# Performance work log

Hardware: AMD Instinct MI355X
Metric: run time of the kernel (lower is better)

## Reference

```python
import jax, jax.numpy as jnp
import numpy as np
import math

L, C, H, FF, V, T, B = 12, 768, 12, 3072, 50257, 512, 4
D = C // H  # head dim = 64


def _layernorm(x, w, b, eps=1e-5):
    m = x.mean(-1, keepdims=True)
    v = ((x - m) ** 2).mean(-1, keepdims=True)
    return (x - m) / jnp.sqrt(v + eps) * w + b


def _gelu(x):
    # tanh-approximate GELU exactly as in the torch module
    return 0.5 * x * (1.0 + jnp.tanh(math.sqrt(2.0 / math.pi) * (x + 0.044715 * x ** 3)))


def setup_inputs() -> dict:
    key = jax.random.key(0)
    ks = jax.random.split(key, 12)
    std = 0.02
    proj_std = 0.02 / math.sqrt(2 * L)
    inp = {
        "idx": jax.random.randint(ks[0], (B, T), 0, V),
        "targets": jax.random.randint(ks[1], (B, T), 0, V),
        "wte": jax.random.normal(ks[2], (V, C), jnp.float32) * std,
        "wpe": jax.random.normal(ks[3], (T, C), jnp.float32) * std,
        "ln1_w": jnp.ones((L, C), jnp.float32),
        "ln1_b": jnp.zeros((L, C), jnp.float32),
        "attn_w": jax.random.normal(ks[4], (L, C, 3 * C), jnp.float32) * std,
        "attn_b": jnp.zeros((L, 3 * C), jnp.float32),
        "attnp_w": jax.random.normal(ks[5], (L, C, C), jnp.float32) * proj_std,
        "attnp_b": jnp.zeros((L, C), jnp.float32),
        "ln2_w": jnp.ones((L, C), jnp.float32),
        "ln2_b": jnp.zeros((L, C), jnp.float32),
        "fc_w": jax.random.normal(ks[6], (L, C, FF), jnp.float32) * std,
        "fc_b": jnp.zeros((L, FF), jnp.float32),
        "fcp_w": jax.random.normal(ks[7], (L, FF, C), jnp.float32) * proj_std,
        "fcp_b": jnp.zeros((L, C), jnp.float32),
        "lnf_w": jnp.ones((C,), jnp.float32),
        "lnf_b": jnp.zeros((C,), jnp.float32),
        "lm_w": jax.random.normal(ks[8], (C, V), jnp.float32) * std,  # lm_head.weight.T
    }
    return inp


def _gpt_forward(idx, targets, wte, wpe, ln1_w, ln1_b, attn_w, attn_b,
                 attnp_w, attnp_b, ln2_w, ln2_b, fc_w, fc_b, fcp_w, fcp_b,
                 lnf_w, lnf_b, lm_w):
    b, t = idx.shape
    x = wte[idx] + wpe[:t][None]  # [B,T,C]
    causal = jnp.tril(jnp.ones((t, t), bool))  # [T,T]
    neg_inf = jnp.float32(-jnp.inf)

    def block(x, p):
        l1w, l1b, aw, ab, pw, pb, l2w, l2b, fw, fb, qw, qb = p
        h = _layernorm(x, l1w, l1b)
        qkv = h @ aw + ab  # [B,T,3C]
        q, k, v = jnp.split(qkv, 3, axis=-1)
        q = q.reshape(b, t, H, D).transpose(0, 2, 1, 3)  # [B,H,T,D]
        k = k.reshape(b, t, H, D).transpose(0, 2, 1, 3)
        v = v.reshape(b, t, H, D).transpose(0, 2, 1, 3)
        att = jnp.einsum('bhqd,bhkd->bhqk', q, k) * (1.0 / math.sqrt(D))
        att = jnp.where(causal, att, neg_inf)
        att = jax.nn.softmax(att, axis=-1)
        y = jnp.einsum('bhqk,bhkd->bhqd', att, v)  # [B,H,T,D]
        y = y.transpose(0, 2, 1, 3).reshape(b, t, C)
        x = x + (y @ pw + pb)
        h2 = _layernorm(x, l2w, l2b)
        x = x + (_gelu(h2 @ fw + fb) @ qw + qb)
        return x, None

    params = (ln1_w, ln1_b, attn_w, attn_b, attnp_w, attnp_b,
              ln2_w, ln2_b, fc_w, fc_b, fcp_w, fcp_b)
    x, _ = jax.lax.scan(block, x, params)
    x = _layernorm(x, lnf_w, lnf_b)
    logits = x @ lm_w  # [B,T,V]

    # cross_entropy with ignore_index=-100
    logp = jax.nn.log_softmax(logits, axis=-1)
    tgt = targets.reshape(-1)
    valid = (tgt != -100)
    safe_tgt = jnp.where(valid, tgt, 0)
    nll = -jnp.take_along_axis(logp.reshape(-1, logits.shape[-1]),
                               safe_tgt[:, None], axis=1)[:, 0]
    loss = jnp.sum(nll * valid) / jnp.maximum(jnp.sum(valid), 1)
    return logits, loss


def reference(idx, targets, wte, wpe, ln1_w, ln1_b, attn_w, attn_b,
              attnp_w, attnp_b, ln2_w, ln2_b, fc_w, fc_b, fcp_w, fcp_b,
              lnf_w, lnf_b, lm_w):
    return _gpt_forward(idx, targets, wte, wpe, ln1_w, ln1_b, attn_w, attn_b,
                        attnp_w, attnp_b, ln2_w, ln2_b, fc_w, fc_b,
                        fcp_w, fcp_b, lnf_w, lnf_b, lm_w)
```

## Files before the change

kernel.cpp:

```cpp
#include <hip/hip_runtime.h>
#include <hip/hip_bf16.h>
#include <math.h>

#define L_ 12
#define C_ 768
#define H_ 12
#define FF_ 3072
#define V_ 50257
#define VP2_ 50432
#define T_ 512
#define B_ 4
#define D_ 64
#define M_ (B_*T_)
#define BH_ (B_*H_)
#define NPAN_LM 197

typedef __attribute__((ext_vector_type(8))) short short8;
typedef __attribute__((ext_vector_type(4))) float f32x4;
typedef __attribute__((ext_vector_type(8))) unsigned short us8;
typedef __attribute__((ext_vector_type(4))) unsigned short us4;

__device__ __forceinline__ float bf2f(unsigned short u) {
    return __uint_as_float(((unsigned)u) << 16);
}
__device__ __forceinline__ unsigned short f2bf(float f) {
    unsigned u = __float_as_uint(f);
    unsigned r = u + 0x7fff + ((u >> 16) & 1);
    return (unsigned short)(r >> 16);
}

__device__ __forceinline__ void transpose_tile(
    const float* __restrict__ W, __hip_bfloat16* __restrict__ WT,
    int K, int N, int Npad, int bx, int by, int bz)
{
    __shared__ float tile[64][65];
    const float* Wl = W + (size_t)bz * K * N;
    __hip_bfloat16* WTl = WT + (size_t)bz * Npad * K;
    int k0 = by * 64, n0 = bx * 64;
    int tid = threadIdx.x;
    int tn = tid & 63, tk4 = tid >> 6;
#pragma unroll 4
    for (int i = 0; i < 16; ++i) {
        int k = tk4 * 16 + i;
        int n = n0 + tn;
        tile[k][tn] = (n < N) ? Wl[(size_t)(k0 + k) * N + n] : 0.f;
    }
    __syncthreads();
#pragma unroll
    for (int i = 0; i < 2; ++i) {
        int p = tid + i * 256;
        int n = p >> 3;
        int k8 = (p & 7) * 8;
        us8 v;
#pragma unroll
        for (int e = 0; e < 8; ++e) v[e] = f2bf(tile[k8 + e][n]);
        *(us8*)((unsigned short*)WTl + (size_t)(n0 + n) * K + k0 + k8) = v;
    }
}

__global__ __launch_bounds__(256) void transpose_all_kernel(
    const float* W0, __hip_bfloat16* T0,
    const float* W1, __hip_bfloat16* T1,
    const float* W2, __hip_bfloat16* T2,
    const float* W3, __hip_bfloat16* T3,
    const float* W4, __hip_bfloat16* T4)
{
    int bid = blockIdx.x;
    if (bid < 5184) {
        int bx = bid % 36, r = bid / 36;
        transpose_tile(W0, T0, C_, 3 * C_, 3 * C_, bx, r % 12, r / 12);
    } else if (bid < 6912) {
        int lb = bid - 5184;
        int bx = lb % 12, r = lb / 12;
        transpose_tile(W1, T1, C_, C_, C_, bx, r % 12, r / 12);
    } else if (bid < 13824) {
        int lb = bid - 6912;
        int bx = lb % 48, r = lb / 48;
        transpose_tile(W2, T2, C_, FF_, FF_, bx, r % 12, r / 12);
    } else if (bid < 20736) {
        int lb = bid - 13824;
        int bx = lb % 12, r = lb / 12;
        transpose_tile(W3, T3, FF_, C_, C_, bx, r % 48, r / 48);
    } else {
        int lb = bid - 20736;
        int bx = lb % 788, by = lb / 788;
        transpose_tile(W4, T4, C_, V_, VP2_, bx, by, 0);
    }
}

__global__ __launch_bounds__(256) void embed_kernel(
    const int* __restrict__ idx, const float* __restrict__ wte,
    const float* __restrict__ wpe, float* __restrict__ x, int total4)
{
    int i = blockIdx.x * blockDim.x + threadIdx.x;
    if (i >= total4) return;
    const int CQ = C_ / 4;
    int c4 = (i % CQ) * 4;
    int row = i / CQ;
    int t = row % T_;
    f32x4 a = *(const f32x4*)(wte + (size_t)idx[row] * C_ + c4);
    f32x4 b = *(const f32x4*)(wpe + (size_t)t * C_ + c4);
    *(f32x4*)(x + (size_t)row * C_ + c4) = a + b;
}

__global__ __launch_bounds__(256) void layernorm_kernel(
    const float* __restrict__ x, const float* __restrict__ w, const float* __restrict__ b,
    __hip_bfloat16* __restrict__ out)
{
    int wv = threadIdx.x >> 6, lane = threadIdx.x & 63;
    int row = blockIdx.x * 4 + wv;
    const float* xr = x + (size_t)row * C_;
    f32x4 v[3];
    float s = 0.f;
#pragma unroll
    for (int j = 0; j < 3; ++j) {
        v[j] = *(const f32x4*)(xr + j * 256 + lane * 4);
        s += v[j][0] + v[j][1] + v[j][2] + v[j][3];
    }
#pragma unroll
    for (int off = 32; off; off >>= 1) s += __shfl_xor(s, off, 64);
    float mean = s * (1.f / (float)C_);
    float var = 0.f;
#pragma unroll
    for (int j = 0; j < 3; ++j)
#pragma unroll
        for (int e = 0; e < 4; ++e) { float d = v[j][e] - mean; var += d * d; }
#pragma unroll
    for (int off = 32; off; off >>= 1) var += __shfl_xor(var, off, 64);
    float rstd = rsqrtf(var * (1.f / (float)C_) + 1e-5f);
    unsigned short* o = (unsigned short*)out + (size_t)row * C_;
#pragma unroll
    for (int j = 0; j < 3; ++j) {
        int c0 = j * 256 + lane * 4;
        f32x4 wv4 = *(const f32x4*)(w + c0);
        f32x4 bv4 = *(const f32x4*)(b + c0);
        us4 u;
#pragma unroll
        for (int e = 0; e < 4; ++e)
            u[e] = f2bf((v[j][e] - mean) * rstd * wv4[e] + bv4[e]);
        *(us4*)(o + c0) = u;
    }
}

template<int MT, int NT, int WM, int WN, int BUFS, int SPLITK,
         int OUTBF, int GELU, int RESID, int LOSSP, int QKVPACK, int ATOMIC, int REPACK>
__global__ __launch_bounds__(64 * WM * WN) void mfma_gemm(
    const __hip_bfloat16* __restrict__ A,
    const __hip_bfloat16* __restrict__ Bt,
    const float* __restrict__ bias,
    const float* __restrict__ resid,
    void* __restrict__ Cout,
    int M, int N, int K, int NB,
    float* __restrict__ lpart, int NPAN,
    unsigned short* __restrict__ Qp, unsigned short* __restrict__ Kp,
    unsigned short* __restrict__ Vt)
{
    constexpr int NTHREADS = 64 * WM * WN;
    constexpr int MPAN = M_ / MT;
    constexpr int MFR = MT / (16 * WM);
    constexpr int AL = (MT * 4) / NTHREADS;
    constexpr int BL = (NT * 4) / NTHREADS;
    constexpr int LOADS = AL + BL;
    constexpr int SMEM_STAGE = BUFS * (MT + NT) * 32 * 2;
    constexpr int SMEM_LS = (LOSSP && !REPACK) ? WN * MT * 4 : 4;
    constexpr int SMEM_RPK = REPACK ? 64 * 264 * 4 : 0;
    constexpr int SMEM_TOT = (SMEM_STAGE + SMEM_LS) > SMEM_RPK ? (SMEM_STAGE + SMEM_LS) : SMEM_RPK;

    int nwg = NB * MPAN * SPLITK;
    int orig = blockIdx.x;
    int xcd = orig & 7;
    int q = nwg >> 3, rr_ = nwg & 7;
    int wgid = (xcd < rr_ ? xcd * (q + 1) : rr_ * (q + 1) + (xcd - rr_) * q) + (orig >> 3);
    int chunk = wgid / (NB * MPAN);
    int rem = wgid % (NB * MPAN);
    int npan = rem / MPAN, mpan = rem % MPAN;
    int m0 = mpan * MT, n0 = npan * NT;
    int KC = K / SPLITK;
    int kbase = chunk * KC;

    __shared__ char smem[SMEM_TOT];
    __hip_bfloat16* AsB = (__hip_bfloat16*)smem;
    __hip_bfloat16* BsB = (__hip_bfloat16*)(smem + BUFS * MT * 32 * 2);
    float* Lsum = (float*)(smem + SMEM_STAGE);
    float* tileF = (float*)smem;
    int tid = threadIdx.x;
    int lane = tid & 63, w = tid >> 6;
    int wn = w % WN, wm = w / WN;
    int lrow = lane & 15, g = lane >> 4;
    f32x4 acc[MFR][4] = {};

    const __hip_bfloat16* Ab = A + (size_t)m0 * K + kbase;
    const __hip_bfloat16* Bb = Bt + (size_t)n0 * K + kbase;

    auto stage = [&](int buf, int k0) {
#pragma unroll
        for (int i = 0; i < AL; ++i) {
            int c = tid + i * NTHREADS;
            int row = c >> 2, s = c & 3;
            int l = (s - (row >> 1)) & 3;
            __builtin_amdgcn_global_load_lds(
                (const __attribute__((address_space(1))) void*)(Ab + (size_t)row * K + k0 + l * 8),
                (__attribute__((address_space(3))) void*)(&AsB[buf * MT * 32 + c * 8]), 16, 0, 0);
        }
#pragma unroll
        for (int i = 0; i < BL; ++i) {
            int c = tid + i * NTHREADS;
            int row = c >> 2, s = c & 3;
            int l = (s - (row >> 1)) & 3;
            __builtin_amdgcn_global_load_lds(
                (const __attribute__((address_space(1))) void*)(Bb + (size_t)row * K + k0 + l * 8),
                (__attribute__((address_space(3))) void*)(&BsB[buf * NT * 32 + c * 8]), 16, 0, 0);
        }
    };
    auto do_tile = [&](int buf) {
        short8 a[MFR], b[4];
#pragma unroll
        for (int i = 0; i < MFR; ++i) {
            int row = wm * (MT / WM) + i * 16 + lrow;
            int s = (g + (row >> 1)) & 3;
            a[i] = *(const short8*)&AsB[buf * MT * 32 + row * 32 + s * 8];
        }
#pragma unroll
        for (int j = 0; j < 4; ++j) {
            int row = wn * 64 + j * 16 + lrow;
            int s = (g + (row >> 1)) & 3;
            b[j] = *(const short8*)&BsB[buf * NT * 32 + row * 32 + s * 8];
        }
        asm volatile("s_waitcnt lgkmcnt(0)" ::: "memory");
        __builtin_amdgcn_sched_barrier(0);
        __builtin_amdgcn_s_setprio(1);
#pragma unroll
        for (int i = 0; i < MFR; ++i)
#pragma unroll
            for (int j = 0; j < 4; ++j)
                acc[i][j] = __builtin_amdgcn_mfma_f32_16x16x32_bf16(a[i], b[j], acc[i][j], 0, 0, 0);
        __builtin_amdgcn_s_setprio(0);
    };

    int nk = KC >> 5;
#pragma unroll
    for (int i = 0; i < BUFS - 1; ++i) stage(i, i << 5);
    for (int t = 0; t < nk; ++t) {
        int ahead = nk - 1 - t;
        if (ahead > BUFS - 2) ahead = BUFS - 2;
        if (ahead == 1) {
            if constexpr (LOADS == 3) asm volatile("s_waitcnt vmcnt(3)" ::: "memory");
            else                      asm volatile("s_waitcnt vmcnt(4)" ::: "memory");
        } else if (ahead >= 2) {
            if constexpr (LOADS == 3) asm volatile("s_waitcnt vmcnt(6)" ::: "memory");
            else                      asm volatile("s_waitcnt vmcnt(8)" ::: "memory");
        } else {
            asm volatile("s_waitcnt vmcnt(0)" ::: "memory");
        }
        __builtin_amdgcn_s_barrier();
        if (t + BUFS - 1 < nk) stage((t + BUFS - 1) % BUFS, (t + BUFS - 1) << 5);
        do_tile(t % BUFS);
    }

    int r0 = g * 4;
    if constexpr (REPACK) {
        float* logitsF = (float*)Cout;
        __syncthreads();
#pragma unroll
        for (int half = 0; half < 2; ++half) {
            if (wm == half) {
#pragma unroll
                for (int i = 0; i < MFR; ++i)
#pragma unroll
                    for (int j = 0; j < 4; ++j)
#pragma unroll
                        for (int r = 0; r < 4; ++r)
                            tileF[(i * 16 + r0 + r) * 264 + wn * 64 + j * 16 + lrow] = acc[i][j][r];
            }
            __syncthreads();
#pragma unroll
            for (int it = 0; it < 64 / (NTHREADS / 64); ++it) {
                int rw = it * (NTHREADS / 64) + (tid >> 6);
                int grow = m0 + half * 64 + rw;
                float ss = 0.f;
#pragma unroll
                for (int e = 0; e < 4; ++e) {
                    int cl = (tid & 63) + e * 64;
                    float v = tileF[rw * 264 + cl];
                    int gcol = n0 + cl;
                    if (gcol < V_) {
                        logitsF[(size_t)grow * V_ + gcol] = v;
                        ss += __expf(v);
                    }
                }
#pragma unroll
                for (int d2 = 1; d2 < 64; d2 <<= 1) ss += __shfl_xor(ss, d2, 64);
                if ((tid & 63) == 0) lpart[(size_t)grow * NPAN + npan] = ss;
            }
            __syncthreads();
        }
        return;
    }
    if (QKVPACK) {
        int which = n0 / 768;
#pragma unroll
        for (int i = 0; i < MFR; ++i) {
#pragma unroll
            for (int j = 0; j < 4; ++j) {
                int col = n0 + wn * 64 + j * 16 + lrow;
                float bv = bias ? bias[col] : 0.f;
                int cc = col - which * 768;
                int hh = cc >> 6, d = cc & 63;
                int row0 = m0 + wm * (MT / WM) + i * 16 + r0;
                int bb = row0 >> 9, tt0 = row0 & (T_ - 1);
                size_t bh = (size_t)bb * H_ + hh;
                if (which == 2) {
                    us4 u;
#pragma unroll
                    for (int r = 0; r < 4; ++r) u[r] = f2bf(acc[i][j][r] + bv);
                    *(us4*)(Vt + (bh * 64 + d) * T_ + tt0) = u;
                } else {
                    unsigned short* dst = (which == 0) ? Qp : Kp;
#pragma unroll
                    for (int r = 0; r < 4; ++r)
                        dst[(bh * T_ + tt0 + r) * 64 + d] = f2bf(acc[i][j][r] + bv);
                }
            }
        }
    } else {
#pragma unroll
        for (int i = 0; i < MFR; ++i) {
#pragma unroll
            for (int j = 0; j < 4; ++j) {
                int col = n0 + wn * 64 + j * 16 + lrow;
                if (col >= N) continue;
                float bv = (bias && (SPLITK == 1 || chunk == 0)) ? bias[col] : 0.f;
#pragma unroll
                for (int r = 0; r < 4; ++r) {
                    int row = m0 + wm * (MT / WM) + i * 16 + r0 + r;
                    float v = acc[i][j][r] + bv;
                    if (GELU) {
                        float t = 0.7978845608028654f * (v + 0.044715f * v * v * v);
                        v = 0.5f * v * (1.f + tanhf(t));
                    }
                    if (RESID) v += resid[(size_t)row * N + col];
                    if (ATOMIC) {
                        atomicAdd(&((float*)Cout)[(size_t)row * N + col], v);
                    } else if (OUTBF) {
                        ((unsigned short*)Cout)[(size_t)row * N + col] = f2bf(v);
                    } else {
                        ((float*)Cout)[(size_t)row * N + col] = v;
                    }
                }
            }
        }
    }
    if constexpr (LOSSP && !REPACK) {
#pragma unroll
        for (int i = 0; i < MFR; ++i) {
#pragma unroll
            for (int r = 0; r < 4; ++r) {
                float ss = 0.f;
#pragma unroll
                for (int j = 0; j < 4; ++j) {
                    int col = n0 + wn * 64 + j * 16 + lrow;
                    if (col < V_) ss += __expf(acc[i][j][r]);
                }
#pragma unroll
                for (int d2 = 1; d2 < 16; d2 <<= 1) ss += __shfl_xor(ss, d2, 64);
                if ((lane & 15) == 0) {
                    int rloc = wm * (MT / WM) + i * 16 + g * 4 + r;
                    Lsum[wn * MT + rloc] = ss;
                }
            }
        }
        __syncthreads();
        if (tid < MT) {
            float ss = Lsum[tid];
#pragma unroll
            for (int ww = 1; ww < WN; ++ww) ss += Lsum[ww * MT + tid];
            lpart[(size_t)(m0 + tid) * NPAN + npan] = ss;
        }
    }
}

__global__ __launch_bounds__(256) void flash_attn_kernel(
    const unsigned short* __restrict__ Qp, const unsigned short* __restrict__ Kp,
    const unsigned short* __restrict__ Vt, unsigned short* __restrict__ y)
{
    int bid = blockIdx.x;
    int xcd = bid & 7;
    int s_ = bid >> 3;
    int bh = xcd * 6 + (s_ % 6);
    int qg = 7 - s_ / 6;
    int b = bh / H_, h = bh % H_;
    int tid = threadIdx.x;
    int w = tid >> 6;
    int lane = tid & 63;
    int c = lane & 15, g = lane >> 4;
    int q0 = (qg * 4 + w) * 16;

    const unsigned short* Qb = Qp + ((size_t)bh * T_ + q0) * 64;
    const unsigned short* Kb = Kp + (size_t)bh * T_ * 64;
    const unsigned short* Vb = Vt + (size_t)bh * 64 * T_;

    short8 qf0 = *(const short8*)(Qb + (size_t)c * 64 + g * 8);
    short8 qf1 = *(const short8*)(Qb + (size_t)c * 64 + 32 + g * 8);

    f32x4 o[4] = {};
    float mrow[4], lrow[4];
#pragma unroll
    for (int r = 0; r < 4; ++r) { mrow[r] = -1e30f; lrow[r] = 0.f; }

    __shared__ unsigned short P_lds[4][16 * 40];

    auto qk_tile = [&](int kv0, f32x4& t0, f32x4& t1) {
        t0 = (f32x4){0.f, 0.f, 0.f, 0.f};
        t1 = (f32x4){0.f, 0.f, 0.f, 0.f};
        const unsigned short* Kt0 = Kb + (size_t)(kv0 + c) * 64;
        short8 b0 = *(const short8*)(Kt0 + g * 8);
        short8 b1 = *(const short8*)(Kt0 + 32 + g * 8);
        const unsigned short* Kt1 = Kb + (size_t)(kv0 + 16 + c) * 64;
        short8 b2 = *(const short8*)(Kt1 + g * 8);
        short8 b3 = *(const short8*)(Kt1 + 32 + g * 8);
        __builtin_amdgcn_s_setprio(1);
        t0 = __builtin_amdgcn_mfma_f32_16x16x32_bf16(qf0, b0, t0, 0, 0, 0);
        t0 = __builtin_amdgcn_mfma_f32_16x16x32_bf16(qf1, b1, t0, 0, 0, 0);
        t1 = __builtin_amdgcn_mfma_f32_16x16x32_bf16(qf0, b2, t1, 0, 0, 0);
        t1 = __builtin_amdgcn_mfma_f32_16x16x32_bf16(qf1, b3, t1, 0, 0, 0);
        __builtin_amdgcn_s_setprio(0);
    };

    int ntiles = q0 / 32 + 1;
    f32x4 sN0, sN1;
    qk_tile(0, sN0, sN1);
    for (int t = 0; t < ntiles; ++t) {
        int kv0 = t * 32;
        f32x4 s0 = sN0, s1 = sN1;
        if (t + 1 < ntiles) qk_tile(kv0 + 32, sN0, sN1);
        if (kv0 + 32 > q0) {
#pragma unroll
            for (int r = 0; r < 4; ++r) {
                int qq = q0 + g * 4 + r;
                float v0 = s0[r] * 0.125f;
                float v1 = s1[r] * 0.125f;
                s0[r] = (kv0 + c <= qq) ? v0 : -1e30f;
                s1[r] = (kv0 + 16 + c <= qq) ? v1 : -1e30f;
            }
        } else {
#pragma unroll
            for (int r = 0; r < 4; ++r) { s0[r] *= 0.125f; s1[r] *= 0.125f; }
        }
        float pmax[4];
#pragma unroll
        for (int r = 0; r < 4; ++r) pmax[r] = fmaxf(s0[r], s1[r]);
#pragma unroll
        for (int d2 = 1; d2 < 16; d2 <<= 1)
#pragma unroll
            for (int r = 0; r < 4; ++r) pmax[r] = fmaxf(pmax[r], __shfl_xor(pmax[r], d2, 64));
        float scl[4], psum[4];
#pragma unroll
        for (int r = 0; r < 4; ++r) {
            float mnew = fmaxf(mrow[r], pmax[r]);
            scl[r] = __expf(mrow[r] - mnew);
            mrow[r] = mnew;
            s0[r] = __expf(s0[r] - mnew);
            s1[r] = __expf(s1[r] - mnew);
            psum[r] = s0[r] + s1[r];
        }
#pragma unroll
        for (int d2 = 1; d2 < 16; d2 <<= 1)
#pragma unroll
            for (int r = 0; r < 4; ++r) psum[r] += __shfl_xor(psum[r], d2, 64);
#pragma unroll
        for (int r = 0; r < 4; ++r) lrow[r] = lrow[r] * scl[r] + psum[r];
#pragma unroll
        for (int j = 0; j < 4; ++j)
#pragma unroll
            for (int r = 0; r < 4; ++r) o[j][r] *= scl[r];
#pragma unroll
        for (int r = 0; r < 4; ++r) {
            P_lds[w][(g * 4 + r) * 40 + c] = f2bf(s0[r]);
            P_lds[w][(g * 4 + r) * 40 + 16 + c] = f2bf(s1[r]);
        }
        asm volatile("s_waitcnt lgkmcnt(0)" ::: "memory");
        __builtin_amdgcn_sched_barrier(0);
        short8 pf = *(const short8*)&P_lds[w][c * 40 + g * 8];
        asm volatile("s_waitcnt lgkmcnt(0)" ::: "memory");
        asm volatile("" ::: "memory");
        __builtin_amdgcn_s_setprio(1);
#pragma unroll
        for (int j = 0; j < 4; ++j) {
            short8 vf = *(const short8*)(Vb + (size_t)(j * 16 + c) * T_ + kv0 + g * 8);
            o[j] = __builtin_amdgcn_mfma_f32_16x16x32_bf16(pf, vf, o[j], 0, 0, 0);
        }
        __builtin_amdgcn_s_setprio(0);
    }
    unsigned short* yb = y + ((size_t)(b * T_ + q0)) * C_ + h * 64;
#pragma unroll
    for (int r = 0; r < 4; ++r) {
        float inv = 1.f / lrow[r];
#pragma unroll
        for (int j = 0; j < 4; ++j)
            yb[(size_t)(g * 4 + r) * C_ + j * 16 + c] = f2bf(o[j][r] * inv);
    }
}

__global__ __launch_bounds__(256) void loss_reduce_kernel(
    const float* __restrict__ lpart, const float* __restrict__ logits,
    const int* __restrict__ targets, float* __restrict__ rnll, int NPAN)
{
    int row = blockIdx.x;
    const float* pp = lpart + (size_t)row * NPAN;
    int tid = threadIdx.x;
    float s = 0.f;
    for (int j = tid; j < NPAN; j += 256) s += pp[j];
    for (int off = 32; off > 0; off >>= 1) s += __shfl_down(s, off, 64);
    __shared__ float rs[4];
    if ((tid & 63) == 0) rs[tid >> 6] = s;
    __syncthreads();
    if (tid == 0) {
        float S = rs[0] + rs[1] + rs[2] + rs[3];
        int t = targets[row];
        if (t != -100) {
            rnll[row] = -(logits[(size_t)row * V_ + t] - logf(S));
            rnll[M_ + row] = 1.f;
        } else {
            rnll[row] = 0.f;
            rnll[M_ + row] = 0.f;
        }
    }
}

__global__ __launch_bounds__(256) void finalize_loss(
    const float* __restrict__ rnll, float* __restrict__ out)
{
    int tid = threadIdx.x;
    float sn = 0.f, sc = 0.f;
    for (int j = tid; j < M_; j += 256) { sn += rnll[j]; sc += rnll[M_ + j]; }
    for (int off = 32; off > 0; off >>= 1) {
        sn += __shfl_down(sn, off, 64);
        sc += __shfl_down(sc, off, 64);
    }
    __shared__ float rn[4], rc[4];
    if ((tid & 63) == 0) { rn[tid >> 6] = sn; rc[tid >> 6] = sc; }
    __syncthreads();
    if (tid == 0) {
        float N = rn[0] + rn[1] + rn[2] + rn[3];
        float Cn = rc[0] + rc[1] + rc[2] + rc[3];
        out[0] = N / fmaxf(Cn, 1.f);
    }
}

extern "C" void kernel_launch(void* const* d_in, const int* in_sizes, int n_in,
                              void* d_out, int out_size, void* d_ws, size_t ws_size,
                              hipStream_t stream)
{
    const int*   idx     = (const int*)d_in[0];
    const int*   targets = (const int*)d_in[1];
    const float* wte     = (const float*)d_in[2];
    const float* wpe     = (const float*)d_in[3];
    const float* ln1_w   = (const float*)d_in[4];
    const float* ln1_b   = (const float*)d_in[5];
    const float* attn_w  = (const float*)d_in[6];
    const float* attn_b  = (const float*)d_in[7];
    const float* attnp_w = (const float*)d_in[8];
    const float* attnp_b = (const float*)d_in[9];
    const float* ln2_w   = (const float*)d_in[10];
    const float* ln2_b   = (const float*)d_in[11];
    const float* fc_w    = (const float*)d_in[12];
    const float* fc_b    = (const float*)d_in[13];
    const float* fcp_w   = (const float*)d_in[14];
    const float* fcp_b   = (const float*)d_in[15];
    const float* lnf_w   = (const float*)d_in[16];
    const float* lnf_b   = (const float*)d_in[17];
    const float* lm_w    = (const float*)d_in[18];

    float* logits = (float*)d_out;
    float* loss   = logits + (size_t)M_ * V_;

    char* p = (char*)d_ws;
    __hip_bfloat16* aw_t = (__hip_bfloat16*)p; p += (size_t)L_ * 3 * C_ * C_ * 2;
    __hip_bfloat16* pw_t = (__hip_bfloat16*)p; p += (size_t)L_ * C_ * C_ * 2;
    __hip_bfloat16* fw_t = (__hip_bfloat16*)p; p += (size_t)L_ * FF_ * C_ * 2;
    __hip_bfloat16* qw_t = (__hip_bfloat16*)p; p += (size_t)L_ * C_ * FF_ * 2;
    __hip_bfloat16* lm_t = (__hip_bfloat16*)p; p += (size_t)VP2_ * C_ * 2;
    float*          x    = (float*)p;          p += (size_t)M_ * C_ * 4;
    __hip_bfloat16* h    = (__hip_bfloat16*)p; p += (size_t)M_ * C_ * 2;
    __hip_bfloat16* y    = (__hip_bfloat16*)p; p += (size_t)M_ * C_ * 2;
    __hip_bfloat16* ff   = (__hip_bfloat16*)p; p += (size_t)M_ * FF_ * 2;
    unsigned short* Qp   = (unsigned short*)p; p += (size_t)BH_ * T_ * 64 * 2;
    unsigned short* Kp   = (unsigned short*)p; p += (size_t)BH_ * T_ * 64 * 2;
    unsigned short* Vt   = (unsigned short*)p; p += (size_t)BH_ * 64 * T_ * 2;
    float*          lpart= (float*)p;          p += (size_t)M_ * NPAN_LM * 4;
    float*          rnll = (float*)p;          p += (size_t)2 * M_ * 4;

    transpose_all_kernel<<<30192, 256, 0, stream>>>(
        attn_w, aw_t, attnp_w, pw_t, fc_w, fw_t, fcp_w, qw_t, lm_w, lm_t);

    {
        int total4 = M_ * C_ / 4;
        embed_kernel<<<(total4 + 255) / 256, 256, 0, stream>>>(idx, wte, wpe, x, total4);
    }

    for (int l = 0; l < L_; ++l) {
        const float* l1w = ln1_w + (size_t)l * C_;
        const float* l1b = ln1_b + (size_t)l * C_;
        const __hip_bfloat16* aw = aw_t + (size_t)l * 3 * C_ * C_;
        const float* ab  = attn_b + (size_t)l * 3 * C_;
        const __hip_bfloat16* pw = pw_t + (size_t)l * C_ * C_;
        const float* pb  = attnp_b + (size_t)l * C_;
        const float* l2w = ln2_w + (size_t)l * C_;
        const float* l2b = ln2_b + (size_t)l * C_;
        const __hip_bfloat16* fw = fw_t + (size_t)l * FF_ * C_;
        const float* fb  = fc_b + (size_t)l * FF_;
        const __hip_bfloat16* qw = qw_t + (size_t)l * C_ * FF_;
        const float* qb  = fcp_b + (size_t)l * C_;

        layernorm_kernel<<<M_ / 4, 256, 0, stream>>>(x, l1w, l1b, h);
        mfma_gemm<64, 128, 2, 2, 3, 1, 0, 0, 0, 0, 1, 0, 0><<<18 * 32, 256, 0, stream>>>(
            h, aw, ab, nullptr, nullptr, M_, 3 * C_, C_, 18, nullptr, 0, Qp, Kp, Vt);
        flash_attn_kernel<<<384, 256, 0, stream>>>(Qp, Kp, Vt, (unsigned short*)y);
        mfma_gemm<64, 128, 2, 2, 3, 2, 0, 0, 0, 0, 0, 1, 0><<<6 * 32 * 2, 256, 0, stream>>>(
            y, pw, pb, nullptr, x, M_, C_, C_, 6, nullptr, 0, nullptr, nullptr, nullptr);
        layernorm_kernel<<<M_ / 4, 256, 0, stream>>>(x, l2w, l2b, h);
        mfma_gemm<64, 128, 2, 2, 3, 1, 1, 1, 0, 0, 0, 0, 0><<<24 * 32, 256, 0, stream>>>(
            h, fw, fb, nullptr, ff, M_, FF_, C_, 24, nullptr, 0, nullptr, nullptr, nullptr);
        mfma_gemm<64, 128, 2, 2, 3, 4, 0, 0, 0, 0, 0, 1, 0><<<6 * 32 * 4, 256, 0, stream>>>(
            ff, qw, qb, nullptr, x, M_, C_, FF_, 6, nullptr, 0, nullptr, nullptr, nullptr);
    }

    layernorm_kernel<<<M_ / 4, 256, 0, stream>>>(x, lnf_w, lnf_b, h);
    mfma_gemm<128, 256, 2, 4, 3, 1, 0, 0, 0, 1, 0, 0, 1><<<NPAN_LM * 16, 512, 0, stream>>>(
        h, lm_t, nullptr, nullptr, logits, M_, V_, C_, NPAN_LM, lpart, NPAN_LM,
        nullptr, nullptr, nullptr);

    loss_reduce_kernel<<<M_, 256, 0, stream>>>(lpart, logits, targets, rnll, NPAN_LM);
    finalize_loss<<<1, 256, 0, stream>>>(rnll, loss);
}
```

Before: 2.081 ms.

## Fuse layernorm into QKV and FC GEMM prologues; add lazy softmax rescale

```diff
diff --git a/kernel.cpp b/kernel.cpp
--- a/kernel.cpp
+++ b/kernel.cpp
@@ -143,7 +143,8 @@
 }
 
 template<int MT, int NT, int WM, int WN, int BUFS, int SPLITK,
-         int OUTBF, int GELU, int RESID, int LOSSP, int QKVPACK, int ATOMIC, int REPACK>
+         int OUTBF, int GELU, int RESID, int LOSSP, int QKVPACK, int ATOMIC, int REPACK,
+         int FUSELN>
 __global__ __launch_bounds__(64 * WM * WN) void mfma_gemm(
     const __hip_bfloat16* __restrict__ A,
     const __hip_bfloat16* __restrict__ Bt,
@@ -153,7 +154,9 @@
     int M, int N, int K, int NB,
     float* __restrict__ lpart, int NPAN,
     unsigned short* __restrict__ Qp, unsigned short* __restrict__ Kp,
-    unsigned short* __restrict__ Vt)
+    unsigned short* __restrict__ Vt,
+    const float* __restrict__ xsrc, const float* __restrict__ lnw,
+    const float* __restrict__ lnb)
 {
     constexpr int NTHREADS = 64 * WM * WN;
     constexpr int MPAN = M_ / MT;
@@ -162,9 +165,11 @@
     constexpr int BL = (NT * 4) / NTHREADS;
     constexpr int LOADS = AL + BL;
     constexpr int SMEM_STAGE = BUFS * (MT + NT) * 32 * 2;
+    constexpr int SMEM_LN = FUSELN ? (2 * C_ * 4 + 2 * MT * 4) : 0;
     constexpr int SMEM_LS = (LOSSP && !REPACK) ? WN * MT * 4 : 4;
     constexpr int SMEM_RPK = REPACK ? 64 * 264 * 4 : 0;
-    constexpr int SMEM_TOT = (SMEM_STAGE + SMEM_LS) > SMEM_RPK ? (SMEM_STAGE + SMEM_LS) : SMEM_RPK;
+    constexpr int SMEM_A = SMEM_STAGE + SMEM_LN + SMEM_LS;
+    constexpr int SMEM_TOT = SMEM_A > SMEM_RPK ? SMEM_A : SMEM_RPK;
 
     int nwg = NB * MPAN * SPLITK;
     int orig = blockIdx.x;
@@ -181,7 +186,11 @@
     __shared__ char smem[SMEM_TOT];
     __hip_bfloat16* AsB = (__hip_bfloat16*)smem;
     __hip_bfloat16* BsB = (__hip_bfloat16*)(smem + BUFS * MT * 32 * 2);
-    float* Lsum = (float*)(smem + SMEM_STAGE);
+    float* lnw_s = (float*)(smem + SMEM_STAGE);
+    float* lnb_s = lnw_s + C_;
+    float* meanS = lnb_s + C_;
+    float* rstdS = meanS + MT;
+    float* Lsum = (float*)(smem + SMEM_STAGE + SMEM_LN);
     float* tileF = (float*)smem;
     int tid = threadIdx.x;
     int lane = tid & 63, w = tid >> 6;
@@ -192,7 +201,18 @@
     const __hip_bfloat16* Ab = A + (size_t)m0 * K + kbase;
     const __hip_bfloat16* Bb = Bt + (size_t)n0 * K + kbase;
 
-    auto stage = [&](int buf, int k0) {
+    auto stageB = [&](int buf, int k0) {
+#pragma unroll
+        for (int i = 0; i < BL; ++i) {
+            int c = tid + i * NTHREADS;
+            int row = c >> 2, s = c & 3;
+            int l = (s - (row >> 1)) & 3;
+            __builtin_amdgcn_global_load_lds(
+                (const __attribute__((address_space(1))) void*)(Bb + (size_t)row * K + k0 + l * 8),
+                (__attribute__((address_space(3))) void*)(&BsB[buf * NT * 32 + c * 8]), 16, 0, 0);
+        }
+    };
+    auto stageA = [&](int buf, int k0) {
 #pragma unroll
         for (int i = 0; i < AL; ++i) {
             int c = tid + i * NTHREADS;
@@ -202,15 +222,6 @@
                 (const __attribute__((address_space(1))) void*)(Ab + (size_t)row * K + k0 + l * 8),
                 (__attribute__((address_space(3))) void*)(&AsB[buf * MT * 32 + c * 8]), 16, 0, 0);
         }
-#pragma unroll
-        for (int i = 0; i < BL; ++i) {
-            int c = tid + i * NTHREADS;
-            int row = c >> 2, s = c & 3;
-            int l = (s - (row >> 1)) & 3;
-            __builtin_amdgcn_global_load_lds(
-                (const __attribute__((address_space(1))) void*)(Bb + (size_t)row * K + k0 + l * 8),
-                (__attribute__((address_space(3))) void*)(&BsB[buf * NT * 32 + c * 8]), 16, 0, 0);
-        }
     };
     auto do_tile = [&](int buf) {
         short8 a[MFR], b[4];
@@ -238,23 +249,93 @@
     };
 
     int nk = KC >> 5;
-#pragma unroll
-    for (int i = 0; i < BUFS - 1; ++i) stage(i, i << 5);
-    for (int t = 0; t < nk; ++t) {
-        int ahead = nk - 1 - t;
-        if (ahead > BUFS - 2) ahead = BUFS - 2;
-        if (ahead == 1) {
-            if constexpr (LOADS == 3) asm volatile("s_waitcnt vmcnt(3)" ::: "memory");
-            else                      asm volatile("s_waitcnt vmcnt(4)" ::: "memory");
-        } else if (ahead >= 2) {
-            if constexpr (LOADS == 3) asm volatile("s_waitcnt vmcnt(6)" ::: "memory");
-            else                      asm volatile("s_waitcnt vmcnt(8)" ::: "memory");
-        } else {
-            asm volatile("s_waitcnt vmcnt(0)" ::: "memory");
-        }
-        __builtin_amdgcn_s_barrier();
-        if (t + BUFS - 1 < nk) stage((t + BUFS - 1) % BUFS, (t + BUFS - 1) << 5);
-        do_tile(t % BUFS);
+    if constexpr (FUSELN) {
+        for (int j = tid; j < C_; j += NTHREADS) { lnw_s[j] = lnw[j]; lnb_s[j] = lnb[j]; }
+        {
+            int wv = w;
+#pragma unroll 1
+            for (int rr = 0; rr < 16; ++rr) {
+                int row = wv * 16 + rr;
+                const float* xr = xsrc + (size_t)(m0 + row) * C_ + lane * 12;
+                f32x4 v0 = *(const f32x4*)(xr);
+                f32x4 v1 = *(const f32x4*)(xr + 4);
+                f32x4 v2 = *(const f32x4*)(xr + 8);
+                float s = v0[0]+v0[1]+v0[2]+v0[3]+v1[0]+v1[1]+v1[2]+v1[3]+v2[0]+v2[1]+v2[2]+v2[3];
+#pragma unroll
+                for (int off = 32; off; off >>= 1) s += __shfl_xor(s, off, 64);
+                float mean = s * (1.f / (float)C_);
+                float var = 0.f;
+#pragma unroll
+                for (int e = 0; e < 4; ++e) { float d0=v0[e]-mean,d1=v1[e]-mean,d2=v2[e]-mean; var += d0*d0+d1*d1+d2*d2; }
+#pragma unroll
+                for (int off = 32; off; off >>= 1) var += __shfl_xor(var, off, 64);
+                if (lane == 0) { meanS[row] = mean; rstdS[row] = rsqrtf(var * (1.f/(float)C_) + 1e-5f); }
+            }
+        }
+        __syncthreads();
+
+        int arow = tid >> 2, akq = tid & 3;
+        const float* xrowp = xsrc + (size_t)(m0 + arow) * C_;
+        int aslot = (akq + (arow >> 1)) & 3;
+        f32x4 xnext0, xnext1, xcur0, xcur1;
+        auto loadx = [&](int u, f32x4& r0, f32x4& r1) {
+            const float* pp = xrowp + u * 32 + akq * 8;
+            r0 = *(const f32x4*)pp;
+            r1 = *(const f32x4*)(pp + 4);
+        };
+        auto writeA = [&](int u, const f32x4& r0, const f32x4& r1) {
+            float mn = meanS[arow], rs = rstdS[arow];
+            int kb = u * 32 + akq * 8;
+            us8 pk;
+#pragma unroll
+            for (int e = 0; e < 4; ++e) {
+                pk[e]     = f2bf((r0[e] - mn) * rs * lnw_s[kb + e]     + lnb_s[kb + e]);
+                pk[e + 4] = f2bf((r1[e] - mn) * rs * lnw_s[kb + 4 + e] + lnb_s[kb + 4 + e]);
+            }
+            *(us8*)&AsB[((u % 3) * MT * 32) + arow * 32 + aslot * 8] = pk;
+        };
+        loadx(0, xnext0, xnext1);
+        stageB(0, 0);
+        asm volatile("s_waitcnt vmcnt(2)" ::: "memory");
+        xcur0 = xnext0; xcur1 = xnext1;
+        loadx(1, xnext0, xnext1);
+        stageB(1, 32);
+        writeA(0, xcur0, xcur1);
+        for (int t = 0; t < nk; ++t) {
+            if (t + 1 < nk) {
+                asm volatile("s_waitcnt vmcnt(2)" ::: "memory");
+            } else {
+                asm volatile("s_waitcnt vmcnt(0)" ::: "memory");
+            }
+            f32x4 c0 = xnext0, c1 = xnext1;
+            if (t + 2 < nk) {
+                loadx(t + 2, xnext0, xnext1);
+                stageB((t + 2) % 3, (t + 2) << 5);
+            }
+            __builtin_amdgcn_s_barrier();
+            if (t + 1 < nk) writeA(t + 1, c0, c1);
+            do_tile(t % 3);
+        }
+    } else {
+#pragma unroll
+        for (int i = 0; i < BUFS - 1; ++i) { stageA(i, i << 5); stageB(i, i << 5); }
+        for (int t = 0; t < nk; ++t) {
+            int ahead = nk - 1 - t;
+            if (ahead > BUFS - 2) ahead = BUFS - 2;
+            if (ahead == 1) {
+                if constexpr (LOADS == 3) asm volatile("s_waitcnt vmcnt(3)" ::: "memory");
+                else                      asm volatile("s_waitcnt vmcnt(4)" ::: "memory");
+            } else if (ahead >= 2) {
+                if constexpr (LOADS == 3) asm volatile("s_waitcnt vmcnt(6)" ::: "memory");
+                else                      asm volatile("s_waitcnt vmcnt(8)" ::: "memory");
+            } else {
+                asm volatile("s_waitcnt vmcnt(0)" ::: "memory");
+            }
+            __builtin_amdgcn_s_barrier();
+            if (t + BUFS - 1 < nk) { stageA((t + BUFS - 1) % BUFS, (t + BUFS - 1) << 5);
+                                     stageB((t + BUFS - 1) % BUFS, (t + BUFS - 1) << 5); }
+            do_tile(t % BUFS);
+        }
     }
 
     int r0 = g * 4;
@@ -453,14 +534,25 @@
         for (int d2 = 1; d2 < 16; d2 <<= 1)
 #pragma unroll
             for (int r = 0; r < 4; ++r) pmax[r] = fmaxf(pmax[r], __shfl_xor(pmax[r], d2, 64));
-        float scl[4], psum[4];
+        bool ok = true;
+#pragma unroll
+        for (int r = 0; r < 4; ++r) ok = ok && (pmax[r] <= mrow[r] + 8.f);
+        if (!__all(ok)) {
+#pragma unroll
+            for (int r = 0; r < 4; ++r) {
+                float mnew = fmaxf(mrow[r], pmax[r]);
+                float scl = __expf(mrow[r] - mnew);
+                mrow[r] = mnew;
+                lrow[r] *= scl;
+#pragma unroll
+                for (int j = 0; j < 4; ++j) o[j][r] *= scl;
+            }
+        }
+        float psum[4];
 #pragma unroll
         for (int r = 0; r < 4; ++r) {
-            float mnew = fmaxf(mrow[r], pmax[r]);
-            scl[r] = __expf(mrow[r] - mnew);
-            mrow[r] = mnew;
-            s0[r] = __expf(s0[r] - mnew);
-            s1[r] = __expf(s1[r] - mnew);
+            s0[r] = __expf(s0[r] - mrow[r]);
+            s1[r] = __expf(s1[r] - mrow[r]);
             psum[r] = s0[r] + s1[r];
         }
 #pragma unroll
@@ -468,11 +560,7 @@
 #pragma unroll
             for (int r = 0; r < 4; ++r) psum[r] += __shfl_xor(psum[r], d2, 64);
 #pragma unroll
-        for (int r = 0; r < 4; ++r) lrow[r] = lrow[r] * scl[r] + psum[r];
-#pragma unroll
-        for (int j = 0; j < 4; ++j)
-#pragma unroll
-            for (int r = 0; r < 4; ++r) o[j][r] *= scl[r];
+        for (int r = 0; r < 4; ++r) lrow[r] += psum[r];
 #pragma unroll
         for (int r = 0; r < 4; ++r) {
             P_lds[w][(g * 4 + r) * 40 + c] = f2bf(s0[r]);
@@ -612,23 +700,25 @@
         const __hip_bfloat16* qw = qw_t + (size_t)l * C_ * FF_;
         const float* qb  = fcp_b + (size_t)l * C_;
 
-        layernorm_kernel<<<M_ / 4, 256, 0, stream>>>(x, l1w, l1b, h);
-        mfma_gemm<64, 128, 2, 2, 3, 1, 0, 0, 0, 0, 1, 0, 0><<<18 * 32, 256, 0, stream>>>(
-            h, aw, ab, nullptr, nullptr, M_, 3 * C_, C_, 18, nullptr, 0, Qp, Kp, Vt);
+        mfma_gemm<64, 128, 2, 2, 3, 1, 0, 0, 0, 0, 1, 0, 0, 1><<<18 * 32, 256, 0, stream>>>(
+            nullptr, aw, ab, nullptr, nullptr, M_, 3 * C_, C_, 18, nullptr, 0, Qp, Kp, Vt,
+            x, l1w, l1b);
         flash_attn_kernel<<<384, 256, 0, stream>>>(Qp, Kp, Vt, (unsigned short*)y);
-        mfma_gemm<64, 128, 2, 2, 3, 2, 0, 0, 0, 0, 0, 1, 0><<<6 * 32 * 2, 256, 0, stream>>>(
-            y, pw, pb, nullptr, x, M_, C_, C_, 6, nullptr, 0, nullptr, nullptr, nullptr);
-        layernorm_kernel<<<M_ / 4, 256, 0, stream>>>(x, l2w, l2b, h);
-        mfma_gemm<64, 128, 2, 2, 3, 1, 1, 1, 0, 0, 0, 0, 0><<<24 * 32, 256, 0, stream>>>(
-            h, fw, fb, nullptr, ff, M_, FF_, C_, 24, nullptr, 0, nullptr, nullptr, nullptr);
-        mfma_gemm<64, 128, 2, 2, 3, 4, 0, 0, 0, 0, 0, 1, 0><<<6 * 32 * 4, 256, 0, stream>>>(
-            ff, qw, qb, nullptr, x, M_, C_, FF_, 6, nullptr, 0, nullptr, nullptr, nullptr);
+        mfma_gemm<64, 128, 2, 2, 3, 2, 0, 0, 0, 0, 0, 1, 0, 0><<<6 * 32 * 2, 256, 0, stream>>>(
+            y, pw, pb, nullptr, x, M_, C_, C_, 6, nullptr, 0, nullptr, nullptr, nullptr,
+            nullptr, nullptr, nullptr);
+        mfma_gemm<64, 128, 2, 2, 3, 1, 1, 1, 0, 0, 0, 0, 0, 1><<<24 * 32, 256, 0, stream>>>(
+            nullptr, fw, fb, nullptr, ff, M_, FF_, C_, 24, nullptr, 0, nullptr, nullptr, nullptr,
+            x, l2w, l2b);
+        mfma_gemm<64, 128, 2, 2, 3, 4, 0, 0, 0, 0, 0, 1, 0, 0><<<6 * 32 * 4, 256, 0, stream>>>(
+            ff, qw, qb, nullptr, x, M_, C_, FF_, 6, nullptr, 0, nullptr, nullptr, nullptr,
+            nullptr, nullptr, nullptr);
     }
 
     layernorm_kernel<<<M_ / 4, 256, 0, stream>>>(x, lnf_w, lnf_b, h);
-    mfma_gemm<128, 256, 2, 4, 3, 1, 0, 0, 0, 1, 0, 0, 1><<<NPAN_LM * 16, 512, 0, stream>>>(
+    mfma_gemm<128, 256, 2, 4, 3, 1, 0, 0, 0, 1, 0, 0, 1, 0><<<NPAN_LM * 16, 512, 0, stream>>>(
         h, lm_t, nullptr, nullptr, logits, M_, V_, C_, NPAN_LM, lpart, NPAN_LM,
-        nullptr, nullptr, nullptr);
+        nullptr, nullptr, nullptr, nullptr, nullptr, nullptr);
 
     loss_reduce_kernel<<<M_, 256, 0, stream>>>(lpart, logits, targets, rnll, NPAN_LM);
     finalize_loss<<<1, 256, 0, stream>>>(rnll, loss);
```

Result: slower. 2.371 ms (+13.9%).
